# Kernel tuning notes

Measured on AMD Instinct MI355X. Metric: run time of the kernel, lower is better.

Reference implementation:

```python
import jax, jax.numpy as jnp
import numpy as np

D_MODEL = 1024
LN_EPS = 1e-5


def setup_inputs() -> dict:
    key = jax.random.key(0)
    k_u, k_b, k_c = jax.random.split(key, 3)
    B, L, D = 8, 4096, D_MODEL
    u = jax.random.normal(k_u, (B, L, D), dtype=jnp.float32)
    # parameters (torch init analogues)
    log_a = jnp.log(jnp.linspace(0.9, 0.99, D, dtype=jnp.float32))
    bound = 1.0 / np.sqrt(D)
    W_b = jax.random.uniform(k_b, (D, D), minval=-bound, maxval=bound, dtype=jnp.float32)
    W_c = jax.random.uniform(k_c, (D, D), minval=-bound, maxval=bound, dtype=jnp.float32)
    gamma = jnp.ones((D,), dtype=jnp.float32)
    beta = jnp.zeros((D,), dtype=jnp.float32)
    return {"u": u, "log_a": log_a, "W_b": W_b, "W_c": W_c, "gamma": gamma, "beta": beta}


def reference(u, log_a, W_b, W_c, gamma, beta):
    # u: [B, L, D]; diagonal LTI SSM: state_t = a * state_{t-1} + (u_t @ W_b^T)
    B, L, D = u.shape
    a = jnp.exp(log_a)  # [D]
    u_b = jnp.einsum('bld,ed->ble', u, W_b)  # batched b-projection over all timesteps

    def step(state, ub_t):
        state = a * state + ub_t
        return state, state

    init = jnp.zeros((B, D), dtype=u.dtype)
    _, states = jax.lax.scan(step, init, jnp.swapaxes(u_b, 0, 1))  # [L, B, D]
    states = jnp.swapaxes(states, 0, 1)  # [B, L, D]

    y = jnp.einsum('bld,ed->ble', states, W_c)  # c-projection batched over time

    # LayerNorm over last dim
    mean = jnp.mean(y, axis=-1, keepdims=True)
    var = jnp.mean(jnp.square(y - mean), axis=-1, keepdims=True)
    return gamma * (y - mean) * jax.lax.rsqrt(var + LN_EPS) + beta
```

## Files before the change

### kernel.cpp

```cpp
#include <hip/hip_runtime.h>
#include <hip/hip_bf16.h>
#include <math.h>

#define B_SZ 8
#define L_SZ 4096
#define D_SZ 1024
#define CHT  64
#define NCH  (L_SZ / CHT)

typedef __bf16 bf16_t;
typedef bf16_t bf16x8 __attribute__((ext_vector_type(8)));
typedef bf16_t bf16x4 __attribute__((ext_vector_type(4)));
typedef float  f32x4  __attribute__((ext_vector_type(4)));

#define BM 256
#define BN 128
#define BK 64
#define NT (1024 / BK)
#define BUFB 49152
#define EP_P 68

__device__ __forceinline__ void gld16(const void* g, void* l) {
  __builtin_amdgcn_global_load_lds(
      (const __attribute__((address_space(1))) void*)g,
      (__attribute__((address_space(3))) void*)l, 16, 0, 0);
}

template<int MODE>
__global__ __launch_bounds__(512, 2)
void gemm256(const bf16_t* __restrict__ A, const bf16_t* __restrict__ Wt,
             bf16_t* __restrict__ Cg, const float* __restrict__ pw,
             float* __restrict__ cf) {
  __shared__ __align__(16) char smem[3 * BUFB];
  const int tid  = threadIdx.x;
  const int lane = tid & 63;
  const int wave = tid >> 6;
  const int wm = wave >> 1, wn = wave & 1;
  const int fr = lane & 15, g = lane >> 4;

  const int flat = (blockIdx.x & 7) * 128 + (blockIdx.x >> 3);
  const int bx = flat & 7, by = flat >> 3;
  const int brow = by * BM, bcol = bx * BN;

  const int sr = lane >> 3;
  const int sc = (lane & 7) ^ sr;
  const bf16_t* a0 = A  + (size_t)(brow + wave * 8 + sr) * 1024 + sc * 8;
  const bf16_t* b0 = Wt + (size_t)(bcol + wave * 8 + sr) * 1024 + sc * 8;

  const int c0 = ((g)     ^ (fr & 7)) << 4;
  const int c1 = ((4 + g) ^ (fr & 7)) << 4;
  const int arowB = (wm * 64 + fr) * 128;
  const int browB = (wn * 64 + fr) * 128;

  f32x4 acc[4][4] = {};

#define STAGE(BU, T) { \
    char* d_ = smem + (BU) * BUFB + wave * 1024; \
    const size_t ko_ = (size_t)(T) * BK; \
    gld16(a0 + ko_, d_); \
    gld16(a0 + (size_t)64 * 1024 + ko_, d_ + 8192); \
    gld16(a0 + (size_t)128 * 1024 + ko_, d_ + 16384); \
    gld16(a0 + (size_t)192 * 1024 + ko_, d_ + 24576); \
    gld16(b0 + ko_, d_ + 32768); \
    gld16(b0 + (size_t)64 * 1024 + ko_, d_ + 40960); \
  }

  STAGE(0, 0)
  STAGE(1, 1)
  asm volatile("s_waitcnt vmcnt(6)" ::: "memory");
  __builtin_amdgcn_s_barrier();
  asm volatile("" ::: "memory");

  int bu = 0, bs = 2;
  for (int t = 0; t < NT; ++t) {
    const char* aB = smem + bu * BUFB;
    const char* bB = aB + 32768;
    bf16x8 af[4][2], bfv[4][2];
#pragma unroll
    for (int mi = 0; mi < 4; ++mi) {
      af[mi][0] = *(const bf16x8*)(aB + arowB + mi * 2048 + c0);
      af[mi][1] = *(const bf16x8*)(aB + arowB + mi * 2048 + c1);
    }
#pragma unroll
    for (int ni = 0; ni < 4; ++ni) {
      bfv[ni][0] = *(const bf16x8*)(bB + browB + ni * 2048 + c0);
      bfv[ni][1] = *(const bf16x8*)(bB + browB + ni * 2048 + c1);
    }
    if (t + 2 < NT) STAGE(bs, t + 2)
    __builtin_amdgcn_s_setprio(1);
#pragma unroll
    for (int mi = 0; mi < 4; ++mi)
#pragma unroll
      for (int ni = 0; ni < 4; ++ni) {
        acc[mi][ni] = __builtin_amdgcn_mfma_f32_16x16x32_bf16(af[mi][0], bfv[ni][0], acc[mi][ni], 0, 0, 0);
        acc[mi][ni] = __builtin_amdgcn_mfma_f32_16x16x32_bf16(af[mi][1], bfv[ni][1], acc[mi][ni], 0, 0, 0);
      }
    __builtin_amdgcn_s_setprio(0);
    if (t + 2 < NT) asm volatile("s_waitcnt vmcnt(6)" ::: "memory");
    else            asm volatile("s_waitcnt vmcnt(0)" ::: "memory");
    __builtin_amdgcn_s_barrier();
    asm volatile("" ::: "memory");
    bu = (bu == 2) ? 0 : bu + 1;
    bs = (bs == 2) ? 0 : bs + 1;
  }
#undef STAGE

  __syncthreads();
  float* strip = (float*)smem;
  const int bb  = by >> 4;
  const int cg0 = (by & 15) * 4;
#pragma unroll 1
  for (int q = 0; q < 2; ++q) {
    if (wn == q) {
#pragma unroll
      for (int mi = 0; mi < 4; ++mi)
#pragma unroll
        for (int ni = 0; ni < 4; ++ni)
#pragma unroll
          for (int r = 0; r < 4; ++r)
            strip[(wm * 64 + mi * 16 + g * 4 + r) * EP_P + ni * 16 + fr] = acc[mi][ni][r];
    }
    __syncthreads();
    if constexpr (MODE == 0) {
      if (tid < 256) {
        const int col = tid & 63;
        const int ch  = tid >> 6;
        const int d   = bcol + q * 64 + col;
        const float a = pw[d];
        float s = 0.f;
#pragma unroll 1
        for (int grp = 0; grp < 4; ++grp) {
          float v[16];
#pragma unroll
          for (int u = 0; u < 16; ++u) v[u] = strip[(ch * 64 + grp * 16 + u) * EP_P + col];
#pragma unroll
          for (int u = 0; u < 16; ++u) { s = a * s + v[u]; v[u] = s; }
#pragma unroll
          for (int u = 0; u < 16; ++u) strip[(ch * 64 + grp * 16 + u) * EP_P + col] = v[u];
        }
        cf[((size_t)(bb * NCH + cg0 + ch)) * D_SZ + d] = s;
      }
      __syncthreads();
    }
#pragma unroll
    for (int j = 0; j < 4; ++j) {
      const int u = j * 512 + tid;
      const int row = u >> 3;
      const int cu = (u & 7) * 8;
      f32x4 lo = *(const f32x4*)&strip[row * EP_P + cu];
      f32x4 hi = *(const f32x4*)&strip[row * EP_P + cu + 4];
      bf16x8 h;
#pragma unroll
      for (int jj = 0; jj < 4; ++jj) { h[jj] = (bf16_t)lo[jj]; h[4 + jj] = (bf16_t)hi[jj]; }
      *(bf16x8*)&Cg[(size_t)(brow + row) * 1024 + bcol + q * 64 + cu] = h;
    }
    __syncthreads();
  }
}

__global__ __launch_bounds__(256)
void conv_bf16_k(const float* __restrict__ src, bf16_t* __restrict__ dst, int n) {
  int i = (blockIdx.x * 256 + threadIdx.x) * 4;
  const int stride = gridDim.x * 256 * 4;
  for (; i < n; i += stride) {
    f32x4 v = *(const f32x4*)(src + i);
    bf16x4 h;
#pragma unroll
    for (int j = 0; j < 4; ++j) h[j] = (bf16_t)v[j];
    *(bf16x4*)(dst + i) = h;
  }
}

__global__ __launch_bounds__(256)
void pow_k(const float* __restrict__ log_a, float* __restrict__ pw) {
  const int t = blockIdx.x;
  const int d = threadIdx.x * 4;
#pragma unroll
  for (int j = 0; j < 4; ++j)
    pw[t * D_SZ + d + j] = expf(log_a[d + j] * (float)(t + 1));
}

__global__ __launch_bounds__(256)
void scan_carry_k(const float* __restrict__ log_a, float* __restrict__ cf) {
  const int d = blockIdx.x * 256 + threadIdx.x;
  const int b = blockIdx.y;
  const float aT = expf(log_a[d] * (float)CHT);
  float s = 0.f;
  for (int c = 0; c < NCH; ++c) {
    const size_t idx = ((size_t)(b * NCH + c)) * D_SZ + d;
    s = aT * s + cf[idx];
    cf[idx] = s;
  }
}

__global__ __launch_bounds__(128)
void scan_apply_k(const bf16_t* __restrict__ xb16, const float* __restrict__ pw,
                  const float* __restrict__ cf, bf16_t* __restrict__ xs16) {
  const int d8 = threadIdx.x * 8;
  const int l = blockIdx.x;
  const int b = blockIdx.y;
  const int c = l >> 6;
  const int t = l & (CHT - 1);
  const size_t idx = ((size_t)(b * L_SZ + l)) * D_SZ + d8;
  bf16x8 hv = *(const bf16x8*)(xb16 + idx);
  float s[8];
#pragma unroll
  for (int j = 0; j < 8; ++j) s[j] = (float)hv[j];
  if (c > 0) {
    f32x4 p0  = *(const f32x4*)(pw + t * D_SZ + d8);
    f32x4 p1  = *(const f32x4*)(pw + t * D_SZ + d8 + 4);
    const float* cb = cf + ((size_t)(b * NCH + (c - 1))) * D_SZ + d8;
    f32x4 v0 = *(const f32x4*)cb;
    f32x4 v1 = *(const f32x4*)(cb + 4);
#pragma unroll
    for (int j = 0; j < 4; ++j) { s[j] += p0[j] * v0[j]; s[4 + j] += p1[j] * v1[j]; }
  }
  bf16x8 h;
#pragma unroll
  for (int j = 0; j < 8; ++j) h[j] = (bf16_t)s[j];
  *(bf16x8*)(xs16 + idx) = h;
}

__global__ __launch_bounds__(256)
void ln_k(const bf16_t* __restrict__ y, const float* __restrict__ gamma,
          const float* __restrict__ beta, float* __restrict__ out) {
  const size_t row = blockIdx.x;
  const int tid = threadIdx.x;
  bf16x4 h = *(const bf16x4*)(y + row * D_SZ + tid * 4);
  float v[4];
#pragma unroll
  for (int j = 0; j < 4; ++j) v[j] = (float)h[j];
  float s  = v[0] + v[1] + v[2] + v[3];
  float sq = v[0] * v[0] + v[1] * v[1] + v[2] * v[2] + v[3] * v[3];
#pragma unroll
  for (int off = 32; off; off >>= 1) {
    s  += __shfl_down(s, off);
    sq += __shfl_down(sq, off);
  }
  __shared__ float red[8];
  const int wid = tid >> 6;
  if ((tid & 63) == 0) { red[wid] = s; red[4 + wid] = sq; }
  __syncthreads();
  s  = red[0] + red[1] + red[2] + red[3];
  sq = red[4] + red[5] + red[6] + red[7];
  const float mean = s * (1.f / D_SZ);
  const float var  = sq * (1.f / D_SZ) - mean * mean;
  const float inv  = rsqrtf(var + 1e-5f);
  f32x4 gm = *(const f32x4*)(gamma + tid * 4);
  f32x4 bt = *(const f32x4*)(beta  + tid * 4);
  f32x4 o;
#pragma unroll
  for (int j = 0; j < 4; ++j) o[j] = (v[j] - mean) * inv * gm[j] + bt[j];
  *(f32x4*)(out + row * D_SZ + tid * 4) = o;
}

extern "C" void kernel_launch(void* const* d_in, const int* in_sizes, int n_in,
                              void* d_out, int out_size, void* d_ws, size_t ws_size,
                              hipStream_t stream) {
  const float* u     = (const float*)d_in[0];
  const float* log_a = (const float*)d_in[1];
  const float* W_b   = (const float*)d_in[2];
  const float* W_c   = (const float*)d_in[3];
  const float* gamma = (const float*)d_in[4];
  const float* beta  = (const float*)d_in[5];
  float* out = (float*)d_out;

  const size_t NBLD = (size_t)B_SZ * L_SZ * D_SZ;
  bf16_t* u16  = (bf16_t*)d_ws;
  bf16_t* xb16 = u16 + NBLD;
  bf16_t* wb16 = xb16 + NBLD;
  bf16_t* wc16 = wb16 + (size_t)D_SZ * D_SZ;
  float*  cf   = (float*)(wc16 + (size_t)D_SZ * D_SZ);
  float*  pw   = cf + (size_t)B_SZ * NCH * D_SZ;
  bf16_t* xs16 = u16;
  bf16_t* y16  = xb16;

  const int nblk = (B_SZ * L_SZ / BM) * (D_SZ / BN);

  conv_bf16_k<<<2048, 256, 0, stream>>>(u, u16, (int)NBLD);
  conv_bf16_k<<<512, 256, 0, stream>>>(W_b, wb16, D_SZ * D_SZ);
  conv_bf16_k<<<512, 256, 0, stream>>>(W_c, wc16, D_SZ * D_SZ);
  pow_k<<<CHT, 256, 0, stream>>>(log_a, pw);

  gemm256<0><<<nblk, 512, 0, stream>>>(u16, wb16, xb16, pw, cf);
  scan_carry_k<<<dim3(D_SZ / 256, B_SZ), 256, 0, stream>>>(log_a, cf);
  scan_apply_k<<<dim3(L_SZ, B_SZ), 128, 0, stream>>>(xb16, pw, cf, xs16);
  gemm256<1><<<nblk, 512, 0, stream>>>(xs16, wc16, y16, nullptr, nullptr);
  ln_k<<<B_SZ * L_SZ, 256, 0, stream>>>(y16, gamma, beta, out);
}
```

Measured before the change: 267.2 us.

## Split GEMM main loop into two phases interleaving LDS reads, prefetch and MFMA

Each K-iteration of the bf16 MFMA GEMM is split into two halves. The first half reads part of the A fragments and issues the A-tile prefetch, then runs half the MFMAs. The second half reads the remaining A fragments and issues the B-tile prefetch, then runs the other MFMAs. The aim is to spread global-to-LDS and LDS-read traffic across the compute phase with a ping-pong style schedule, at the cost of extra workgroup barriers per iteration.

```diff
diff --git a/kernel.cpp b/kernel.cpp
--- a/kernel.cpp
+++ b/kernel.cpp
@@ -54,19 +54,23 @@
 
   f32x4 acc[4][4] = {};
 
-#define STAGE(BU, T) { \
+#define STAGE_A(BU, T) { \
     char* d_ = smem + (BU) * BUFB + wave * 1024; \
     const size_t ko_ = (size_t)(T) * BK; \
     gld16(a0 + ko_, d_); \
     gld16(a0 + (size_t)64 * 1024 + ko_, d_ + 8192); \
     gld16(a0 + (size_t)128 * 1024 + ko_, d_ + 16384); \
     gld16(a0 + (size_t)192 * 1024 + ko_, d_ + 24576); \
+  }
+#define STAGE_B(BU, T) { \
+    char* d_ = smem + (BU) * BUFB + wave * 1024; \
+    const size_t ko_ = (size_t)(T) * BK; \
     gld16(b0 + ko_, d_ + 32768); \
     gld16(b0 + (size_t)64 * 1024 + ko_, d_ + 40960); \
   }
 
-  STAGE(0, 0)
-  STAGE(1, 1)
+  STAGE_A(0, 0) STAGE_B(0, 0)
+  STAGE_A(1, 1) STAGE_B(1, 1)
   asm volatile("s_waitcnt vmcnt(6)" ::: "memory");
   __builtin_amdgcn_s_barrier();
   asm volatile("" ::: "memory");
@@ -77,7 +81,7 @@
     const char* bB = aB + 32768;
     bf16x8 af[4][2], bfv[4][2];
 #pragma unroll
-    for (int mi = 0; mi < 4; ++mi) {
+    for (int mi = 0; mi < 2; ++mi) {
       af[mi][0] = *(const bf16x8*)(aB + arowB + mi * 2048 + c0);
       af[mi][1] = *(const bf16x8*)(aB + arowB + mi * 2048 + c1);
     }
@@ -86,10 +90,31 @@
       bfv[ni][0] = *(const bf16x8*)(bB + browB + ni * 2048 + c0);
       bfv[ni][1] = *(const bf16x8*)(bB + browB + ni * 2048 + c1);
     }
-    if (t + 2 < NT) STAGE(bs, t + 2)
+    if (t + 2 < NT) STAGE_A(bs, t + 2)
+    __builtin_amdgcn_s_barrier();
+    asm volatile("" ::: "memory");
     __builtin_amdgcn_s_setprio(1);
 #pragma unroll
-    for (int mi = 0; mi < 4; ++mi)
+    for (int mi = 0; mi < 2; ++mi)
+#pragma unroll
+      for (int ni = 0; ni < 4; ++ni) {
+        acc[mi][ni] = __builtin_amdgcn_mfma_f32_16x16x32_bf16(af[mi][0], bfv[ni][0], acc[mi][ni], 0, 0, 0);
+        acc[mi][ni] = __builtin_amdgcn_mfma_f32_16x16x32_bf16(af[mi][1], bfv[ni][1], acc[mi][ni], 0, 0, 0);
+      }
+    __builtin_amdgcn_s_setprio(0);
+    __builtin_amdgcn_s_barrier();
+    asm volatile("" ::: "memory");
+#pragma unroll
+    for (int mi = 2; mi < 4; ++mi) {
+      af[mi][0] = *(const bf16x8*)(aB + arowB + mi * 2048 + c0);
+      af[mi][1] = *(const bf16x8*)(aB + arowB + mi * 2048 + c1);
+    }
+    if (t + 2 < NT) STAGE_B(bs, t + 2)
+    __builtin_amdgcn_s_barrier();
+    asm volatile("" ::: "memory");
+    __builtin_amdgcn_s_setprio(1);
+#pragma unroll
+    for (int mi = 2; mi < 4; ++mi)
 #pragma unroll
       for (int ni = 0; ni < 4; ++ni) {
         acc[mi][ni] = __builtin_amdgcn_mfma_f32_16x16x32_bf16(af[mi][0], bfv[ni][0], acc[mi][ni], 0, 0, 0);
@@ -103,7 +128,8 @@
     bu = (bu == 2) ? 0 : bu + 1;
     bs = (bs == 2) ? 0 : bs + 1;
   }
-#undef STAGE
+#undef STAGE_A
+#undef STAGE_B
 
   __syncthreads();
   float* strip = (float*)smem;
```

Measured after the change: 272.4 us. Within noise of the previous version (+1.9%).

## Enlarge GEMM tile to 256x256 with interleaved double-buffered prefetch phases

Applied to the files above, without the earlier changes.

Switches the bf16 GEMM block tile from 256x128 to 256x256, giving each wave a 128x64 subtile with 8x4 accumulators. The 3-stage ring buffer is replaced by 2-stage double buffering, and the next K-tile's global-to-LDS loads are spread across four MFMA phases separated by barriers. The aim is more reuse of each loaded tile per MFMA and better overlap of loads with compute. It costs more registers and 128KB of LDS per block, which with launch_bounds(512,2) may limit occupancy, and it adds extra barriers per iteration.

```diff
diff --git a/kernel.cpp b/kernel.cpp
--- a/kernel.cpp
+++ b/kernel.cpp
@@ -14,10 +14,9 @@
 typedef float  f32x4  __attribute__((ext_vector_type(4)));
 
 #define BM 256
-#define BN 128
+#define BN 256
 #define BK 64
-#define NT (1024 / BK)
-#define BUFB 49152
+#define NT 16
 #define EP_P 68
 
 __device__ __forceinline__ void gld16(const void* g, void* l) {
@@ -25,100 +24,147 @@
       (const __attribute__((address_space(1))) void*)g,
       (__attribute__((address_space(3))) void*)l, 16, 0, 0);
 }
+
+#define MFMA16(a, b, c) __builtin_amdgcn_mfma_f32_16x16x32_bf16(a, b, c, 0, 0, 0)
 
 template<int MODE>
 __global__ __launch_bounds__(512, 2)
 void gemm256(const bf16_t* __restrict__ A, const bf16_t* __restrict__ Wt,
              bf16_t* __restrict__ Cg, const float* __restrict__ pw,
              float* __restrict__ cf) {
-  __shared__ __align__(16) char smem[3 * BUFB];
+  __shared__ __align__(16) char smem[131072];
   const int tid  = threadIdx.x;
   const int lane = tid & 63;
   const int wave = tid >> 6;
-  const int wm = wave >> 1, wn = wave & 1;
+  const int wm = wave >> 2, wn = wave & 3;
   const int fr = lane & 15, g = lane >> 4;
 
-  const int flat = (blockIdx.x & 7) * 128 + (blockIdx.x >> 3);
-  const int bx = flat & 7, by = flat >> 3;
+  const int flat = (blockIdx.x & 7) * 64 + (blockIdx.x >> 3);
+  const int bx = flat & 3, by = flat >> 2;
   const int brow = by * BM, bcol = bx * BN;
 
-  const int sr = lane >> 3;
-  const int sc = (lane & 7) ^ sr;
-  const bf16_t* a0 = A  + (size_t)(brow + wave * 8 + sr) * 1024 + sc * 8;
-  const bf16_t* b0 = Wt + (size_t)(bcol + wave * 8 + sr) * 1024 + sc * 8;
+  const int srow = lane >> 3;
+  const int sc   = (lane & 7) ^ srow;
+  const bf16_t* aSrc = A  + (size_t)(brow + wave * 8 + srow) * 1024 + sc * 8;
+  const bf16_t* bSrc = Wt + (size_t)(bcol + wave * 8 + srow) * 1024 + sc * 8;
 
   const int c0 = ((g)     ^ (fr & 7)) << 4;
   const int c1 = ((4 + g) ^ (fr & 7)) << 4;
-  const int arowB = (wm * 64 + fr) * 128;
-  const int browB = (wn * 64 + fr) * 128;
-
-  f32x4 acc[4][4] = {};
-
-#define STAGE(BU, T) { \
-    char* d_ = smem + (BU) * BUFB + wave * 1024; \
-    const size_t ko_ = (size_t)(T) * BK; \
-    gld16(a0 + ko_, d_); \
-    gld16(a0 + (size_t)64 * 1024 + ko_, d_ + 8192); \
-    gld16(a0 + (size_t)128 * 1024 + ko_, d_ + 16384); \
-    gld16(a0 + (size_t)192 * 1024 + ko_, d_ + 24576); \
-    gld16(b0 + ko_, d_ + 32768); \
-    gld16(b0 + (size_t)64 * 1024 + ko_, d_ + 40960); \
-  }
-
-  STAGE(0, 0)
-  STAGE(1, 1)
-  asm volatile("s_waitcnt vmcnt(6)" ::: "memory");
+  const int aoff = wm * 16384 + fr * 128;
+  const int boff = 65536 + (wn >> 1) * 16384 + ((wn & 1) * 64 + fr) * 128;
+
+#define STG_A(DB, H, I, T) gld16(aSrc + (size_t)((H) * 128 + (I) * 64) * 1024 + (T) * 64, \
+                                 (DB) + (H) * 16384 + (I) * 8192 + wave * 1024)
+#define STG_B(DB, H, I, T) gld16(bSrc + (size_t)((H) * 128 + (I) * 64) * 1024 + (T) * 64, \
+                                 (DB) + 65536 + (H) * 16384 + (I) * 8192 + wave * 1024)
+
+  f32x4 acc[8][4] = {};
+  bf16x8 af[4][2], bfv[4][2];
+
+  {
+    char* db = smem;
+    STG_A(db, 0, 0, 0); STG_A(db, 0, 1, 0); STG_A(db, 1, 0, 0); STG_A(db, 1, 1, 0);
+    STG_B(db, 0, 0, 0); STG_B(db, 0, 1, 0); STG_B(db, 1, 0, 0); STG_B(db, 1, 1, 0);
+  }
+  asm volatile("s_waitcnt vmcnt(0)" ::: "memory");
   __builtin_amdgcn_s_barrier();
   asm volatile("" ::: "memory");
 
-  int bu = 0, bs = 2;
   for (int t = 0; t < NT; ++t) {
-    const char* aB = smem + bu * BUFB;
-    const char* bB = aB + 32768;
-    bf16x8 af[4][2], bfv[4][2];
-#pragma unroll
-    for (int mi = 0; mi < 4; ++mi) {
-      af[mi][0] = *(const bf16x8*)(aB + arowB + mi * 2048 + c0);
-      af[mi][1] = *(const bf16x8*)(aB + arowB + mi * 2048 + c1);
-    }
-#pragma unroll
-    for (int ni = 0; ni < 4; ++ni) {
-      bfv[ni][0] = *(const bf16x8*)(bB + browB + ni * 2048 + c0);
-      bfv[ni][1] = *(const bf16x8*)(bB + browB + ni * 2048 + c1);
-    }
-    if (t + 2 < NT) STAGE(bs, t + 2)
+    const int s = t & 1;
+    const char* sb = smem + s * 32768;
+    char* db = smem + (s ^ 1) * 32768;
+    const bool pf = (t + 1 < NT);
+
+#pragma unroll
+    for (int m = 0; m < 4; ++m) {
+      af[m][0] = *(const bf16x8*)(sb + aoff + m * 2048 + c0);
+      af[m][1] = *(const bf16x8*)(sb + aoff + m * 2048 + c1);
+    }
+#pragma unroll
+    for (int n = 0; n < 2; ++n) {
+      bfv[n][0] = *(const bf16x8*)(sb + boff + n * 2048 + c0);
+      bfv[n][1] = *(const bf16x8*)(sb + boff + n * 2048 + c1);
+    }
+    if (pf) { STG_A(db, 0, 0, t + 1); STG_A(db, 0, 1, t + 1); }
+    __builtin_amdgcn_s_barrier(); asm volatile("" ::: "memory");
     __builtin_amdgcn_s_setprio(1);
 #pragma unroll
-    for (int mi = 0; mi < 4; ++mi)
-#pragma unroll
-      for (int ni = 0; ni < 4; ++ni) {
-        acc[mi][ni] = __builtin_amdgcn_mfma_f32_16x16x32_bf16(af[mi][0], bfv[ni][0], acc[mi][ni], 0, 0, 0);
-        acc[mi][ni] = __builtin_amdgcn_mfma_f32_16x16x32_bf16(af[mi][1], bfv[ni][1], acc[mi][ni], 0, 0, 0);
+    for (int m = 0; m < 4; ++m)
+#pragma unroll
+      for (int n = 0; n < 2; ++n) {
+        acc[m][n] = MFMA16(af[m][0], bfv[n][0], acc[m][n]);
+        acc[m][n] = MFMA16(af[m][1], bfv[n][1], acc[m][n]);
       }
     __builtin_amdgcn_s_setprio(0);
-    if (t + 2 < NT) asm volatile("s_waitcnt vmcnt(6)" ::: "memory");
-    else            asm volatile("s_waitcnt vmcnt(0)" ::: "memory");
+    __builtin_amdgcn_s_barrier(); asm volatile("" ::: "memory");
+
+#pragma unroll
+    for (int n = 2; n < 4; ++n) {
+      bfv[n][0] = *(const bf16x8*)(sb + boff + n * 2048 + c0);
+      bfv[n][1] = *(const bf16x8*)(sb + boff + n * 2048 + c1);
+    }
+    if (pf) { STG_A(db, 1, 0, t + 1); STG_A(db, 1, 1, t + 1); STG_B(db, 0, 0, t + 1); }
+    __builtin_amdgcn_s_barrier(); asm volatile("" ::: "memory");
+    __builtin_amdgcn_s_setprio(1);
+#pragma unroll
+    for (int m = 0; m < 4; ++m)
+#pragma unroll
+      for (int n = 2; n < 4; ++n) {
+        acc[m][n] = MFMA16(af[m][0], bfv[n][0], acc[m][n]);
+        acc[m][n] = MFMA16(af[m][1], bfv[n][1], acc[m][n]);
+      }
+    __builtin_amdgcn_s_setprio(0);
+    __builtin_amdgcn_s_barrier(); asm volatile("" ::: "memory");
+
+#pragma unroll
+    for (int m = 0; m < 4; ++m) {
+      af[m][0] = *(const bf16x8*)(sb + aoff + (4 + m) * 2048 + c0);
+      af[m][1] = *(const bf16x8*)(sb + aoff + (4 + m) * 2048 + c1);
+    }
+    if (pf) { STG_B(db, 0, 1, t + 1); STG_B(db, 1, 0, t + 1); STG_B(db, 1, 1, t + 1); }
+    __builtin_amdgcn_s_barrier(); asm volatile("" ::: "memory");
+    __builtin_amdgcn_s_setprio(1);
+#pragma unroll
+    for (int m = 0; m < 4; ++m)
+#pragma unroll
+      for (int n = 0; n < 2; ++n) {
+        acc[4 + m][n] = MFMA16(af[m][0], bfv[n][0], acc[4 + m][n]);
+        acc[4 + m][n] = MFMA16(af[m][1], bfv[n][1], acc[4 + m][n]);
+      }
+    __builtin_amdgcn_s_setprio(0);
+    __builtin_amdgcn_s_barrier(); asm volatile("" ::: "memory");
+
+    __builtin_amdgcn_s_setprio(1);
+#pragma unroll
+    for (int m = 0; m < 4; ++m)
+#pragma unroll
+      for (int n = 2; n < 4; ++n) {
+        acc[4 + m][n] = MFMA16(af[m][0], bfv[n][0], acc[4 + m][n]);
+        acc[4 + m][n] = MFMA16(af[m][1], bfv[n][1], acc[4 + m][n]);
+      }
+    __builtin_amdgcn_s_setprio(0);
+    asm volatile("s_waitcnt vmcnt(0)" ::: "memory");
     __builtin_amdgcn_s_barrier();
     asm volatile("" ::: "memory");
-    bu = (bu == 2) ? 0 : bu + 1;
-    bs = (bs == 2) ? 0 : bs + 1;
-  }
-#undef STAGE
+  }
+#undef STG_A
+#undef STG_B
 
   __syncthreads();
   float* strip = (float*)smem;
   const int bb  = by >> 4;
   const int cg0 = (by & 15) * 4;
 #pragma unroll 1
-  for (int q = 0; q < 2; ++q) {
+  for (int q = 0; q < 4; ++q) {
     if (wn == q) {
 #pragma unroll
-      for (int mi = 0; mi < 4; ++mi)
+      for (int mi = 0; mi < 8; ++mi)
 #pragma unroll
         for (int ni = 0; ni < 4; ++ni)
 #pragma unroll
           for (int r = 0; r < 4; ++r)
-            strip[(wm * 64 + mi * 16 + g * 4 + r) * EP_P + ni * 16 + fr] = acc[mi][ni][r];
+            strip[(wm * 128 + mi * 16 + g * 4 + r) * EP_P + ni * 16 + fr] = acc[mi][ni][r];
     }
     __syncthreads();
     if constexpr (MODE == 0) {
```

After: 253.5 us, median of 2. 5.1% less time.

## Widen GEMM tile to 256x256 with BK=32 and 2x4 wave grid

Applied to the files above, without the earlier changes.

Changes the GEMM block tile from 256x128 to 256x256, halving K-step depth to 32 and rearranging eight waves as 2x4 with each wave computing 128x64 (8x4 MFMA tiles). This raises arithmetic intensity per LDS byte and per global load, and halves the number of blocks that re-read A. It lowers occupancy to one block per CU, doubles accumulator registers, and makes the epilogue loop over four column strips instead of two.

```diff
diff --git a/kernel.cpp b/kernel.cpp
--- a/kernel.cpp
+++ b/kernel.cpp
@@ -14,10 +14,10 @@
 typedef float  f32x4  __attribute__((ext_vector_type(4)));
 
 #define BM 256
-#define BN 128
-#define BK 64
-#define NT (1024 / BK)
-#define BUFB 49152
+#define BN 256
+#define BK 32
+#define NT 32
+#define BUFB 32768
 #define EP_P 68
 
 __device__ __forceinline__ void gld16(const void* g, void* l) {
@@ -26,8 +26,10 @@
       (__attribute__((address_space(3))) void*)l, 16, 0, 0);
 }
 
+#define MFMA16(a, b, c) __builtin_amdgcn_mfma_f32_16x16x32_bf16(a, b, c, 0, 0, 0)
+
 template<int MODE>
-__global__ __launch_bounds__(512, 2)
+__global__ __launch_bounds__(512, 1)
 void gemm256(const bf16_t* __restrict__ A, const bf16_t* __restrict__ Wt,
              bf16_t* __restrict__ Cg, const float* __restrict__ pw,
              float* __restrict__ cf) {
@@ -35,90 +37,80 @@
   const int tid  = threadIdx.x;
   const int lane = tid & 63;
   const int wave = tid >> 6;
-  const int wm = wave >> 1, wn = wave & 1;
+  const int wm = wave >> 2, wn = wave & 3;
   const int fr = lane & 15, g = lane >> 4;
 
-  const int flat = (blockIdx.x & 7) * 128 + (blockIdx.x >> 3);
-  const int bx = flat & 7, by = flat >> 3;
+  const int flat = (blockIdx.x & 7) * 64 + (blockIdx.x >> 3);
+  const int bx = flat & 3, by = flat >> 2;
   const int brow = by * BM, bcol = bx * BN;
 
-  const int sr = lane >> 3;
-  const int sc = (lane & 7) ^ sr;
-  const bf16_t* a0 = A  + (size_t)(brow + wave * 8 + sr) * 1024 + sc * 8;
-  const bf16_t* b0 = Wt + (size_t)(bcol + wave * 8 + sr) * 1024 + sc * 8;
-
-  const int c0 = ((g)     ^ (fr & 7)) << 4;
-  const int c1 = ((4 + g) ^ (fr & 7)) << 4;
-  const int arowB = (wm * 64 + fr) * 128;
-  const int browB = (wn * 64 + fr) * 128;
-
-  f32x4 acc[4][4] = {};
-
-#define STAGE(BU, T) { \
-    char* d_ = smem + (BU) * BUFB + wave * 1024; \
+  const int srow4 = lane >> 2;
+  const int sch   = (lane & 3) ^ (srow4 & 3);
+  const bf16_t* aSrc = A  + (size_t)(brow + wave * 32 + srow4) * 1024 + sch * 8;
+  const bf16_t* bSrc = Wt + (size_t)(bcol + wave * 32 + srow4) * 1024 + sch * 8;
+
+  const int c_rd = ((g ^ (fr & 3)) << 4);
+  const int aoff = wm * 8192 + fr * 64;
+  const int boff = 16384 + wn * 4096 + fr * 64;
+
+#define STG(DB, T) { \
+    char* d_ = (DB) + wave * 2048; \
     const size_t ko_ = (size_t)(T) * BK; \
-    gld16(a0 + ko_, d_); \
-    gld16(a0 + (size_t)64 * 1024 + ko_, d_ + 8192); \
-    gld16(a0 + (size_t)128 * 1024 + ko_, d_ + 16384); \
-    gld16(a0 + (size_t)192 * 1024 + ko_, d_ + 24576); \
-    gld16(b0 + ko_, d_ + 32768); \
-    gld16(b0 + (size_t)64 * 1024 + ko_, d_ + 40960); \
-  }
-
-  STAGE(0, 0)
-  STAGE(1, 1)
-  asm volatile("s_waitcnt vmcnt(6)" ::: "memory");
+    gld16(aSrc + ko_, d_); \
+    gld16(aSrc + (size_t)16 * 1024 + ko_, d_ + 1024); \
+    gld16(bSrc + ko_, d_ + 16384); \
+    gld16(bSrc + (size_t)16 * 1024 + ko_, d_ + 17408); \
+  }
+
+  f32x4 acc[8][4] = {};
+  bf16x8 af[8], bfv[4];
+
+  STG(smem, 0);
+  STG(smem + BUFB, 1);
+  asm volatile("s_waitcnt vmcnt(4)" ::: "memory");
   __builtin_amdgcn_s_barrier();
   asm volatile("" ::: "memory");
 
   int bu = 0, bs = 2;
   for (int t = 0; t < NT; ++t) {
-    const char* aB = smem + bu * BUFB;
-    const char* bB = aB + 32768;
-    bf16x8 af[4][2], bfv[4][2];
-#pragma unroll
-    for (int mi = 0; mi < 4; ++mi) {
-      af[mi][0] = *(const bf16x8*)(aB + arowB + mi * 2048 + c0);
-      af[mi][1] = *(const bf16x8*)(aB + arowB + mi * 2048 + c1);
-    }
-#pragma unroll
-    for (int ni = 0; ni < 4; ++ni) {
-      bfv[ni][0] = *(const bf16x8*)(bB + browB + ni * 2048 + c0);
-      bfv[ni][1] = *(const bf16x8*)(bB + browB + ni * 2048 + c1);
-    }
-    if (t + 2 < NT) STAGE(bs, t + 2)
+    const char* sb = smem + bu * BUFB;
+#pragma unroll
+    for (int m = 0; m < 8; ++m)
+      af[m] = *(const bf16x8*)(sb + aoff + m * 1024 + c_rd);
+#pragma unroll
+    for (int n = 0; n < 4; ++n)
+      bfv[n] = *(const bf16x8*)(sb + boff + n * 1024 + c_rd);
+    if (t + 2 < NT) STG(smem + bs * BUFB, t + 2);
     __builtin_amdgcn_s_setprio(1);
 #pragma unroll
-    for (int mi = 0; mi < 4; ++mi)
-#pragma unroll
-      for (int ni = 0; ni < 4; ++ni) {
-        acc[mi][ni] = __builtin_amdgcn_mfma_f32_16x16x32_bf16(af[mi][0], bfv[ni][0], acc[mi][ni], 0, 0, 0);
-        acc[mi][ni] = __builtin_amdgcn_mfma_f32_16x16x32_bf16(af[mi][1], bfv[ni][1], acc[mi][ni], 0, 0, 0);
-      }
+    for (int m = 0; m < 8; ++m)
+#pragma unroll
+      for (int n = 0; n < 4; ++n)
+        acc[m][n] = MFMA16(af[m], bfv[n], acc[m][n]);
     __builtin_amdgcn_s_setprio(0);
-    if (t + 2 < NT) asm volatile("s_waitcnt vmcnt(6)" ::: "memory");
+    if (t + 2 < NT) asm volatile("s_waitcnt vmcnt(4)" ::: "memory");
     else            asm volatile("s_waitcnt vmcnt(0)" ::: "memory");
     __builtin_amdgcn_s_barrier();
     asm volatile("" ::: "memory");
     bu = (bu == 2) ? 0 : bu + 1;
     bs = (bs == 2) ? 0 : bs + 1;
   }
-#undef STAGE
+#undef STG
 
   __syncthreads();
   float* strip = (float*)smem;
   const int bb  = by >> 4;
   const int cg0 = (by & 15) * 4;
 #pragma unroll 1
-  for (int q = 0; q < 2; ++q) {
+  for (int q = 0; q < 4; ++q) {
     if (wn == q) {
 #pragma unroll
-      for (int mi = 0; mi < 4; ++mi)
+      for (int mi = 0; mi < 8; ++mi)
 #pragma unroll
         for (int ni = 0; ni < 4; ++ni)
 #pragma unroll
           for (int r = 0; r < 4; ++r)
-            strip[(wm * 64 + mi * 16 + g * 4 + r) * EP_P + ni * 16 + fr] = acc[mi][ni][r];
+            strip[(wm * 128 + mi * 16 + g * 4 + r) * EP_P + ni * 16 + fr] = acc[mi][ni][r];
     }
     __syncthreads();
     if constexpr (MODE == 0) {
```

Result: no change. 265.0 us (-0.8%).
